# Kernel optimization log

Hardware: AMD Instinct MI355X
Metric: run time of the kernel (lower is better)

The kernel has to match this reference:

```python
import jax, jax.numpy as jnp
import numpy as np

HIDDEN, DOWN, UP, NH, RHD = 2048, 512, 1024, 16, 64
HEAD_DIM = HIDDEN // NH        # 128 (used only in the score scale)
V_HEAD = UP // NH              # 64
BASE = 10000.0


def _rope(q):
    # q: [bs, heads, seq, d] with even d. Faithful to the torch module,
    # including its swapped sin/cos cache names.
    d = q.shape[-1]
    seq = q.shape[2]
    theta = BASE ** (-jnp.arange(0, d, 2, dtype=jnp.float32) / d)      # [d/2]
    pos = jnp.arange(seq, dtype=jnp.float32)[:, None] * theta[None, :]  # [seq, d/2]
    cos_pos = jnp.repeat(jnp.sin(pos), 2, axis=-1)  # torch code: cos_pos = sin(...)
    sin_pos = jnp.repeat(jnp.cos(pos), 2, axis=-1)  # torch code: sin_pos = cos(...)
    q2 = jnp.stack([-q[..., 1::2], q[..., ::2]], axis=-1).reshape(q.shape)
    return q * cos_pos[None, None] + q2 * sin_pos[None, None]


def setup_inputs() -> dict:
    key = jax.random.key(0)
    ks = jax.random.split(key, 12)
    bs, seq = 16, 512

    def lin(k, fan_in, fan_out):
        kw, kb = jax.random.split(k)
        bound = 1.0 / np.sqrt(fan_in)
        W = jax.random.uniform(kw, (fan_in, fan_out), jnp.float32, -bound, bound)
        b = jax.random.uniform(kb, (fan_out,), jnp.float32, -bound, bound)
        return W, b

    x = jax.random.normal(ks[0], (bs, seq, HIDDEN), jnp.float32)
    mask = jax.random.randint(ks[1], (bs, seq), 0, 2, jnp.int32)
    w_dkv, b_dkv = lin(ks[2], HIDDEN, DOWN)
    w_dq, b_dq = lin(ks[3], HIDDEN, DOWN)
    w_uq, b_uq = lin(ks[4], DOWN, UP)
    w_uk, b_uk = lin(ks[5], DOWN, UP)
    w_uv, b_uv = lin(ks[6], DOWN, UP)
    w_qr, b_qr = lin(ks[7], DOWN, RHD * NH)
    w_kr, b_kr = lin(ks[8], DOWN, RHD)
    w_fc, b_fc = lin(ks[9], NH * V_HEAD, HIDDEN)
    return dict(x=x, mask=mask, w_dkv=w_dkv, b_dkv=b_dkv, w_dq=w_dq, b_dq=b_dq,
                w_uq=w_uq, b_uq=b_uq, w_uk=w_uk, b_uk=b_uk, w_uv=w_uv, b_uv=b_uv,
                w_qr=w_qr, b_qr=b_qr, w_kr=w_kr, b_kr=b_kr, w_fc=w_fc, b_fc=b_fc)


def reference(x, mask, w_dkv, b_dkv, w_dq, b_dq, w_uq, b_uq, w_uk, b_uk,
              w_uv, b_uv, w_qr, b_qr, w_kr, b_kr, w_fc, b_fc):
    bs, seq, _ = x.shape
    # latent down-projections
    c_kv = x @ w_dkv + b_dkv                       # [bs, seq, DOWN]
    c_q = x @ w_dq + b_dq                          # [bs, seq, DOWN]
    # content up-projections
    k_c = (c_kv @ w_uk + b_uk).reshape(bs, seq, NH, UP // NH).transpose(0, 2, 1, 3)
    v_c = (c_kv @ w_uv + b_uv).reshape(bs, seq, NH, V_HEAD).transpose(0, 2, 1, 3)
    q_c = (c_q @ w_uq + b_uq).reshape(bs, seq, NH, UP // NH).transpose(0, 2, 1, 3)
    # rope branches
    q_r = (c_q @ w_qr + b_qr).reshape(bs, seq, NH, RHD).transpose(0, 2, 1, 3)
    q_r = _rope(q_r)                               # [bs, NH, seq, RHD]
    k_r = (c_kv @ w_kr + b_kr)[:, None]            # [bs, 1, seq, RHD]
    k_r = _rope(k_r)
    # concat content + rope dims
    q = jnp.concatenate([q_c, q_r], axis=-1)                        # [bs,NH,seq,UP/NH+RHD]
    k = jnp.concatenate([k_c, jnp.broadcast_to(k_r, (bs, NH, seq, RHD))], axis=-1)
    scale = 1.0 / (HEAD_DIM ** 0.5 + RHD ** 0.5)
    scores = jnp.einsum('bhqd,bhkd->bhqk', q, k) * scale
    scores = jnp.where(mask[:, None, None, :] == 0, -jnp.inf, scores)
    attn = jax.nn.softmax(scores, axis=-1)
    ctx = jnp.einsum('bhqk,bhkd->bhqd', attn, v_c)                  # [bs,NH,seq,V_HEAD]
    ctx = ctx.transpose(0, 2, 1, 3).reshape(bs, seq, NH * V_HEAD)
    return ctx @ w_fc + b_fc
```

## Files before the change

kernel.cpp:

```cpp
#include <hip/hip_runtime.h>
#include <cstdint>
#include <cmath>

typedef unsigned short u16;
typedef unsigned int   u32;
typedef _Float16 f16x8 __attribute__((ext_vector_type(8)));
typedef float f32x4  __attribute__((ext_vector_type(4)));

#define MFMAH(a, b, c) __builtin_amdgcn_mfma_f32_16x16x32_f16((a), (b), (c), 0, 0, 0)

__device__ __forceinline__ u16 f2h(float f) {
  _Float16 h = (_Float16)f;
  return __builtin_bit_cast(u16, h);
}
__device__ __forceinline__ float h2f(u16 u) {
  return (float)__builtin_bit_cast(_Float16, u);
}
__device__ __forceinline__ float fexp2(float x) { return __builtin_amdgcn_exp2f(x); }
__device__ __forceinline__ void async16(const void* g, void* l) {
  __builtin_amdgcn_global_load_lds((const __attribute__((address_space(1))) u32*)g,
                                   (__attribute__((address_space(3))) u32*)l, 16, 0, 0);
}

__global__ void stab_kernel(float2* __restrict__ stab) {
  int idx = blockIdx.x * 256 + threadIdx.x;
  int s = idx >> 5, i = idx & 31;
  float theta = exp2f((float)i * (-13.287712379549449f / 32.0f));
  float ang = (float)s * theta;
  stab[idx] = make_float2(sinf(ang), cosf(ang));
}

__global__ void biascat_kernel(const float* __restrict__ buq, const float* __restrict__ bqr,
                               const float* __restrict__ buk, const float* __restrict__ buv,
                               const float* __restrict__ bkr,
                               float* __restrict__ biasQ, float* __restrict__ biasKV) {
  int idx = blockIdx.x * 256 + threadIdx.x;
  if (idx < 2048) biasQ[idx] = (idx < 1024) ? buq[idx] : bqr[idx - 1024];
  int j = idx - 2048;
  if (j >= 0 && j < 2176)
    biasKV[j] = (j < 1024) ? buk[j]
              : (j < 2048) ? buv[j - 1024]
              : (j < 2112) ? bkr[j - 2048] : 0.f;
}

__global__ void convert_x_kernel(const float* __restrict__ x, u16* __restrict__ xh, int n4) {
  int i = blockIdx.x * blockDim.x + threadIdx.x;
  if (i >= n4) return;
  float4 v = reinterpret_cast<const float4*>(x)[i];
  uint2 p;
  p.x = (u32)f2h(v.x) | ((u32)f2h(v.y) << 16);
  p.y = (u32)f2h(v.z) | ((u32)f2h(v.w) << 16);
  reinterpret_cast<uint2*>(xh)[i] = p;
}

template <int NOUT>
__global__ void wtrans_kernel(const float* __restrict__ W, int N,
                              u16* __restrict__ Thi, u16* __restrict__ Tlo,
                              int row_off, int dst_ld) {
  __shared__ float tile[32][33];
  int k0 = blockIdx.x * 32, n0 = blockIdx.y * 32;
  int tx = threadIdx.x & 31, ty = threadIdx.x >> 5;
#pragma unroll
  for (int i = 0; i < 32; i += 8)
    tile[ty + i][tx] = W[(size_t)(k0 + ty + i) * N + n0 + tx];
  __syncthreads();
#pragma unroll
  for (int i = 0; i < 32; i += 8) {
    float v = tile[tx][ty + i];
    size_t o = (size_t)(row_off + n0 + ty + i) * dst_ld + k0 + tx;
    u16 h = f2h(v);
    Thi[o] = h;
    if constexpr (NOUT == 2) Tlo[o] = f2h(v - h2f(h));
  }
}

template <int MODE, int TERMS>
__global__ __launch_bounds__(256, TERMS == 2 ? 3 : 4) void gemmh_kernel(
    const u16* __restrict__ Ah, int lda,
    const u16* __restrict__ Bhi, const u16* __restrict__ Blo, int ldb,
    const float* __restrict__ bias, const float* __restrict__ bias2, int bsplit,
    void* __restrict__ out0, void* __restrict__ out1, void* __restrict__ out2,
    const float2* __restrict__ stab, int N, int K, int ldc) {
  __shared__ u16 lA[128 * 64];
  __shared__ u16 lB[TERMS][128 * 64];
  const int tid = threadIdx.x;
  const int wave = tid >> 6, lane = tid & 63;
  const int lrow = lane & 15, kgrp = lane >> 4;
  const int nwg = gridDim.x * gridDim.y;
  const int orig = blockIdx.y * gridDim.x + blockIdx.x;
  const int swz = (orig & 7) * (nwg >> 3) + (orig >> 3);
  const int bm = (swz % gridDim.x) * 128, bn = (swz / gridDim.x) * 128;
  const int wm = (wave >> 1) * 64, wn = (wave & 1) * 64;
  const int srow = lane >> 3, sg = lane & 7;

  f32x4 acc[4][4];
  const f32x4 zero = {0.f, 0.f, 0.f, 0.f};
#pragma unroll
  for (int i = 0; i < 4; ++i)
#pragma unroll
    for (int j = 0; j < 4; ++j) acc[i][j] = zero;

  for (int kt = 0; kt < K; kt += 64) {
#pragma unroll
    for (int ii = 0; ii < 4; ++ii) {
      int inst = wave * 4 + ii;
      int row = inst * 8 + srow;
      int koff = kt + ((sg ^ (row & 7)) << 3);
      async16(Ah + (size_t)(bm + row) * lda + koff, &lA[inst * 512]);
      int brow = bn + row;
      if (brow > N - 1) brow = N - 1;
      async16(Bhi + (size_t)brow * ldb + koff, &lB[0][inst * 512]);
      if constexpr (TERMS == 2)
        async16(Blo + (size_t)brow * ldb + koff, &lB[TERMS - 1][inst * 512]);
    }
    asm volatile("s_waitcnt vmcnt(0)" ::: "memory");
    __syncthreads();

#pragma unroll
    for (int ks = 0; ks < 2; ++ks) {
      f16x8 ah[4], b0v[4], b1v[4];
#pragma unroll
      for (int mi = 0; mi < 4; ++mi) {
        int row = wm + mi * 16 + lrow;
        int off = row * 128 + ((ks * 64 + kgrp * 16) ^ ((row & 7) << 4));
        ah[mi] = *(const f16x8*)((const char*)lA + off);
      }
#pragma unroll
      for (int ni = 0; ni < 4; ++ni) {
        int row = wn + ni * 16 + lrow;
        int off = row * 128 + ((ks * 64 + kgrp * 16) ^ ((row & 7) << 4));
        b0v[ni] = *(const f16x8*)((const char*)lB[0] + off);
        if constexpr (TERMS == 2)
          b1v[ni] = *(const f16x8*)((const char*)lB[TERMS - 1] + off);
      }
#pragma unroll
      for (int mi = 0; mi < 4; ++mi)
#pragma unroll
        for (int ni = 0; ni < 4; ++ni) {
          acc[mi][ni] = MFMAH(ah[mi], b0v[ni], acc[mi][ni]);
          if constexpr (TERMS == 2)
            acc[mi][ni] = MFMAH(ah[mi], b1v[ni], acc[mi][ni]);
        }
    }
    __syncthreads();
  }

#pragma unroll
  for (int mi = 0; mi < 4; ++mi) {
#pragma unroll
    for (int ni = 0; ni < 4; ++ni) {
      int col = bn + wn + ni * 16 + lrow;
      float bv = (col < bsplit) ? bias[col] : bias2[col - bsplit];
      int row0 = bm + wm + mi * 16 + kgrp * 4;
      if constexpr (MODE == 0) {
#pragma unroll
        for (int r = 0; r < 4; ++r)
          ((float*)out0)[(size_t)(row0 + r) * ldc + col] = acc[mi][ni][r] + bv;
      } else if constexpr (MODE == 3) {
#pragma unroll
        for (int r = 0; r < 4; ++r)
          ((u16*)out0)[(size_t)(row0 + r) * ldc + col] = f2h(acc[mi][ni][r] + bv);
      } else if constexpr (MODE == 7) {
        if (col < 1024) {
#pragma unroll
          for (int r = 0; r < 4; ++r) {
            int row = row0 + r;
            ((u16*)out0)[(((size_t)((row >> 9) * 16 + (col >> 6)) * 512 + (row & 511)) << 7)
                         + (col & 63)] = f2h(acc[mi][ni][r] + bv);
          }
        } else {
          int cc = col - 1024, hh = cc >> 6, d = cc & 63, i2 = d >> 1;
          bool odd = d & 1;
#pragma unroll
          for (int r = 0; r < 4; ++r) {
            int row = row0 + r, s = row & 511;
            float vv = acc[mi][ni][r] + bv;
            float p = __shfl_xor(vv, 1, 64);
            float2 t2 = stab[s * 32 + i2];
            float o = odd ? (vv * t2.x + p * t2.y) : (vv * t2.x - p * t2.y);
            ((u16*)out0)[(((size_t)((row >> 9) * 16 + hh) * 512 + (row & 511)) << 7)
                         + 64 + d] = f2h(o);
          }
        }
      } else if constexpr (MODE == 6) {
        if (col < 1024) {
#pragma unroll
          for (int r = 0; r < 4; ++r) {
            int row = row0 + r;
            ((u16*)out0)[(((size_t)((row >> 9) * 16 + (col >> 6)) * 512 + (row & 511)) << 7)
                         + (col & 63)] = f2h(acc[mi][ni][r] + bv);
          }
        } else if (col < 2048) {
          int cc = col - 1024;
          u16 h0 = f2h(acc[mi][ni][0] + bv), h1 = f2h(acc[mi][ni][1] + bv);
          u16 h2 = f2h(acc[mi][ni][2] + bv), h3 = f2h(acc[mi][ni][3] + bv);
          uint2 pk;
          pk.x = (u32)h0 | ((u32)h1 << 16);
          pk.y = (u32)h2 | ((u32)h3 << 16);
          size_t base = ((size_t)((row0 >> 9) * 16 + (cc >> 6)) * 64 + (cc & 63)) * 512
                        + (row0 & 511);
          *reinterpret_cast<uint2*>((u16*)out1 + base) = pk;
        } else {
#pragma unroll
          for (int r = 0; r < 4; ++r)
            ((float*)out2)[(size_t)(row0 + r) * 128 + (col - 2048)] = acc[mi][ni][r] + bv;
        }
      }
    }
  }
}

__global__ void ropek_kernel(const float* __restrict__ kr, const float2* __restrict__ stab,
                             u16* __restrict__ Kb) {
  int idx = blockIdx.x * 256 + threadIdx.x;
  int t = idx >> 5, i = idx & 31;
  float vx = kr[(size_t)t * 128 + 2 * i], vy = kr[(size_t)t * 128 + 2 * i + 1];
  float2 t2 = stab[(t & 511) * 32 + i];
  float o0 = vx * t2.x - vy * t2.y;
  float o1 = vy * t2.x + vx * t2.y;
  u32 pk = (u32)f2h(o0) | ((u32)f2h(o1) << 16);
  int bb = t >> 9, ss = t & 511;
  size_t base = (size_t)bb * 16 * 512 * 128;
#pragma unroll
  for (int hh = 0; hh < 16; ++hh)
    *reinterpret_cast<u32*>(Kb + base + ((size_t)(hh * 512 + ss)) * 128 + 64 + 2 * i) = pk;
}

__global__ __launch_bounds__(256, 3) void attn_kernel(
    const u16* __restrict__ Qb, const u16* __restrict__ Kb, const u16* __restrict__ Vt,
    const int* __restrict__ mask, u16* __restrict__ ctx,
    float scale2) {
  __shared__ u16 sQ[64 * 128];
  __shared__ u16 sK[64 * 128];
  __shared__ u16 sV[64 * 64];
  __shared__ u16 sP[4][1024];
  const int tid = threadIdx.x, wave = tid >> 6, lane = tid & 63;
  const int lrow = lane & 15, kgrp = lane >> 4;
  const int bh = blockIdx.x, b = bh >> 4, h = bh & 15;
  const int q0 = blockIdx.y * 64;
  const size_t qkbase = (size_t)bh * 512 * 128;
  const size_t vbase = (size_t)bh * 64 * 512;
  u16* __restrict__ sPw = sP[wave];

  u32 poff[4][4];
#pragma unroll
  for (int r = 0; r < 4; ++r) {
    int qp = kgrp * 4 + r;
#pragma unroll
    for (int nf = 0; nf < 4; ++nf)
      poff[r][nf] = (u32)((nf >> 1) * 512 + ((((nf & 1) << 1) | (lrow >> 3))) * 128
                          + qp * 8 + (lrow & 7));
  }

  {
    int g = lane & 15, rr = lane >> 4;
#pragma unroll
    for (int ii = 0; ii < 4; ++ii) {
      int inst = wave * 4 + ii;
      int row = inst * 4 + rr;
      int perm = (g & 8) | ((g & 7) ^ (row & 7));
      async16(Qb + qkbase + (size_t)(q0 + row) * 128 + perm * 8, &sQ[inst * 512]);
    }
  }

  const f32x4 zero = {0.f, 0.f, 0.f, 0.f};
  f32x4 O[4];
#pragma unroll
  for (int nf = 0; nf < 4; ++nf) O[nf] = zero;
  float m_run[4], l_part[4];
#pragma unroll
  for (int r = 0; r < 4; ++r) { m_run[r] = -1e30f; l_part[r] = 0.f; }

  for (int kvt = 0; kvt < 8; ++kvt) {
    const int kv0 = kvt * 64;
    {
      int g = lane & 15, rr = lane >> 4;
#pragma unroll
      for (int ii = 0; ii < 4; ++ii) {
        int inst = wave * 4 + ii;
        int row = inst * 4 + rr;
        int perm = (g & 8) | ((g & 7) ^ (row & 7));
        async16(Kb + qkbase + (size_t)(kv0 + row) * 128 + perm * 8, &sK[inst * 512]);
      }
      int g2 = lane & 7, r2 = lane >> 3;
#pragma unroll
      for (int ii = 0; ii < 2; ++ii) {
        int inst = wave * 2 + ii;
        int row = inst * 8 + r2;
        async16(Vt + vbase + (size_t)row * 512 + kv0 + ((g2 ^ (row & 7)) << 3),
                &sV[inst * 512]);
      }
    }
    float mb[4];
#pragma unroll
    for (int nf = 0; nf < 4; ++nf)
      mb[nf] = (mask[b * 512 + kv0 + nf * 16 + lrow] != 0) ? 0.f : -1e30f;

    asm volatile("s_waitcnt vmcnt(0)" ::: "memory");
    __syncthreads();

    f32x4 S[4];
#pragma unroll
    for (int nf = 0; nf < 4; ++nf) S[nf] = zero;
#pragma unroll
    for (int ks = 0; ks < 4; ++ks) {
      int qrow = wave * 16 + lrow;
      int kb = ks * 64 + kgrp * 16;
      f16x8 aq = *(const f16x8*)((const char*)sQ + qrow * 256 + (kb ^ ((qrow & 7) << 4)));
#pragma unroll
      for (int nf = 0; nf < 4; ++nf) {
        int krow = nf * 16 + lrow;
        f16x8 bk = *(const f16x8*)((const char*)sK + krow * 256 + (kb ^ ((krow & 7) << 4)));
        S[nf] = MFMAH(aq, bk, S[nf]);
      }
    }

    float pvv[4][4];
    float tmax[4];
#pragma unroll
    for (int r = 0; r < 4; ++r) tmax[r] = -1e30f;
#pragma unroll
    for (int nf = 0; nf < 4; ++nf) {
#pragma unroll
      for (int r = 0; r < 4; ++r) {
        float v = fmaf(S[nf][r], scale2, mb[nf]);
        pvv[nf][r] = v;
        tmax[r] = fmaxf(tmax[r], v);
      }
    }
#pragma unroll
    for (int r = 0; r < 4; ++r) {
#pragma unroll
      for (int mv = 1; mv < 16; mv <<= 1)
        tmax[r] = fmaxf(tmax[r], __shfl_xor(tmax[r], mv, 64));
    }

    bool grow = (tmax[0] > m_run[0] + 8.f) || (tmax[1] > m_run[1] + 8.f) ||
                (tmax[2] > m_run[2] + 8.f) || (tmax[3] > m_run[3] + 8.f);
    if (__any(grow ? 1 : 0)) {
#pragma unroll
      for (int r = 0; r < 4; ++r) {
        float newm = fmaxf(m_run[r], tmax[r]);
        float sc = fexp2(m_run[r] - newm);
        m_run[r] = newm;
        float ts = 0.f;
#pragma unroll
        for (int nf = 0; nf < 4; ++nf) {
          float pe = fexp2(pvv[nf][r] - newm);
          sPw[poff[r][nf]] = f2h(pe);
          ts += pe;
        }
        l_part[r] = l_part[r] * sc + ts;
#pragma unroll
        for (int nf = 0; nf < 4; ++nf) O[nf][r] *= sc;
      }
    } else {
#pragma unroll
      for (int r = 0; r < 4; ++r) {
        float ts = 0.f;
#pragma unroll
        for (int nf = 0; nf < 4; ++nf) {
          float pe = fexp2(pvv[nf][r] - m_run[r]);
          sPw[poff[r][nf]] = f2h(pe);
          ts += pe;
        }
        l_part[r] += ts;
      }
    }

#pragma unroll
    for (int ks = 0; ks < 2; ++ks) {
      int kb = ks * 64 + kgrp * 16;
      f16x8 ap = *(const f16x8*)((const char*)sPw + ((ks * 64 + kgrp * 16 + lrow) << 4));
#pragma unroll
      for (int nf = 0; nf < 4; ++nf) {
        int vr = nf * 16 + lrow;
        f16x8 bv = *(const f16x8*)((const char*)sV + vr * 128 + (kb ^ ((vr & 7) << 4)));
        O[nf] = MFMAH(ap, bv, O[nf]);
      }
    }
    __syncthreads();
  }

#pragma unroll
  for (int r = 0; r < 4; ++r) {
#pragma unroll
    for (int mv = 1; mv < 16; mv <<= 1) l_part[r] += __shfl_xor(l_part[r], mv, 64);
  }

#pragma unroll
  for (int r = 0; r < 4; ++r) {
    float inv = 1.0f / l_part[r];
    int trow = b * 512 + q0 + wave * 16 + kgrp * 4 + r;
#pragma unroll
    for (int nf = 0; nf < 4; ++nf) {
      int col = h * 64 + nf * 16 + lrow;
      ctx[(size_t)trow * 1024 + col] = f2h(O[nf][r] * inv);
    }
  }
}

extern "C" void kernel_launch(void* const* d_in, const int* in_sizes, int n_in,
                              void* d_out, int out_size, void* d_ws, size_t ws_size,
                              hipStream_t stream) {
  const float* x     = (const float*)d_in[0];
  const int*   mask  = (const int*)d_in[1];
  const float* w_dkv = (const float*)d_in[2];
  const float* b_dkv = (const float*)d_in[3];
  const float* w_dq  = (const float*)d_in[4];
  const float* b_dq  = (const float*)d_in[5];
  const float* w_uq  = (const float*)d_in[6];
  const float* b_uq  = (const float*)d_in[7];
  const float* w_uk  = (const float*)d_in[8];
  const float* b_uk  = (const float*)d_in[9];
  const float* w_uv  = (const float*)d_in[10];
  const float* b_uv  = (const float*)d_in[11];
  const float* w_qr  = (const float*)d_in[12];
  const float* b_qr  = (const float*)d_in[13];
  const float* w_kr  = (const float*)d_in[14];
  const float* b_kr  = (const float*)d_in[15];
  const float* w_fc  = (const float*)d_in[16];
  const float* b_fc  = (const float*)d_in[17];
  float* out = (float*)d_out;

  char* ws = (char*)d_ws;
  size_t off = 0;
  auto alloc = [&](size_t bytes) -> void* {
    void* p = ws + off;
    off += (bytes + 255) & ~(size_t)255;
    return p;
  };
  u16* xh     = (u16*)alloc(33554432);
  u16* WfTh   = (u16*)alloc(4194304);
  u16* WfTl   = (u16*)alloc(4194304);
  u16* WqT    = (u16*)alloc(2097152);
  u16* WkvT   = (u16*)alloc(2228224);
  u16* WfcTh  = (u16*)alloc(4194304);
  u16* WfcTl  = (u16*)alloc(4194304);
  u16* c      = (u16*)alloc(16777216);
  u16* Qb     = (u16*)alloc(33554432);
  u16* Kb     = (u16*)alloc(33554432);
  u16* Vt     = (u16*)alloc(16777216);
  float* krf  = (float*)alloc(4194304);
  float2* stab = (float2*)alloc(131072);
  float* biasQ  = (float*)alloc(8192);
  float* biasKV = (float*)alloc(8704);
  u16* ctx = c;
  (void)ws_size; (void)in_sizes; (void)n_in; (void)out_size;

  const float scale = 1.0f / (sqrtf(128.0f) + sqrtf(64.0f));
  const float scale2 = scale * 1.4426950408889634f;

  stab_kernel<<<64, 256, 0, stream>>>(stab);
  convert_x_kernel<<<16384, 256, 0, stream>>>(x, xh, 4194304);
  biascat_kernel<<<17, 256, 0, stream>>>(b_uq, b_qr, b_uk, b_uv, b_kr, biasQ, biasKV);
  wtrans_kernel<2><<<dim3(64, 16), 256, 0, stream>>>(w_dkv, 512, WfTh, WfTl, 0, 2048);
  wtrans_kernel<2><<<dim3(64, 16), 256, 0, stream>>>(w_dq, 512, WfTh, WfTl, 512, 2048);
  wtrans_kernel<1><<<dim3(16, 32), 256, 0, stream>>>(w_uq, 1024, WqT, nullptr, 0, 512);
  wtrans_kernel<1><<<dim3(16, 32), 256, 0, stream>>>(w_qr, 1024, WqT, nullptr, 1024, 512);
  wtrans_kernel<1><<<dim3(16, 32), 256, 0, stream>>>(w_uk, 1024, WkvT, nullptr, 0, 512);
  wtrans_kernel<1><<<dim3(16, 32), 256, 0, stream>>>(w_uv, 1024, WkvT, nullptr, 1024, 512);
  wtrans_kernel<1><<<dim3(16, 2), 256, 0, stream>>>(w_kr, 64, WkvT, nullptr, 2048, 512);
  wtrans_kernel<2><<<dim3(32, 64), 256, 0, stream>>>(w_fc, 2048, WfcTh, WfcTl, 0, 1024);

  gemmh_kernel<3, 2><<<dim3(64, 8), 256, 0, stream>>>(
      xh, 2048, WfTh, WfTl, 2048, b_dkv, b_dq, 512,
      (void*)c, nullptr, nullptr, nullptr, 1024, 2048, 1024);
  gemmh_kernel<7, 1><<<dim3(64, 16), 256, 0, stream>>>(
      c + 512, 1024, WqT, nullptr, 512, biasQ, biasQ, 2048,
      (void*)Qb, nullptr, nullptr, stab, 2048, 512, 0);
  gemmh_kernel<6, 1><<<dim3(64, 17), 256, 0, stream>>>(
      c, 1024, WkvT, nullptr, 512, biasKV, biasKV, 2176,
      (void*)Kb, (void*)Vt, (void*)krf, nullptr, 2176, 512, 0);

  ropek_kernel<<<1024, 256, 0, stream>>>(krf, stab, Kb);

  attn_kernel<<<dim3(256, 8), 256, 0, stream>>>(Qb, Kb, Vt, mask, ctx, scale2);

  gemmh_kernel<0, 2><<<dim3(64, 16), 256, 0, stream>>>(
      ctx, 1024, WfcTh, WfcTl, 1024, b_fc, b_fc, 2048,
      (void*)out, nullptr, nullptr, nullptr, 2048, 1024, 2048);
}
```

Measured before the change: 458.7 us.

## Keep attention probabilities in registers via transposed S and batch prep launches

```diff
diff --git a/kernel.cpp b/kernel.cpp
--- a/kernel.cpp
+++ b/kernel.cpp
@@ -22,25 +22,25 @@
                                    (__attribute__((address_space(3))) u32*)l, 16, 0, 0);
 }
 
-__global__ void stab_kernel(float2* __restrict__ stab) {
+__global__ void prep_kernel(float2* __restrict__ stab,
+                            const float* __restrict__ buq, const float* __restrict__ bqr,
+                            const float* __restrict__ buk, const float* __restrict__ buv,
+                            const float* __restrict__ bkr,
+                            float* __restrict__ biasQ, float* __restrict__ biasKV) {
   int idx = blockIdx.x * 256 + threadIdx.x;
-  int s = idx >> 5, i = idx & 31;
-  float theta = exp2f((float)i * (-13.287712379549449f / 32.0f));
-  float ang = (float)s * theta;
-  stab[idx] = make_float2(sinf(ang), cosf(ang));
-}
-
-__global__ void biascat_kernel(const float* __restrict__ buq, const float* __restrict__ bqr,
-                               const float* __restrict__ buk, const float* __restrict__ buv,
-                               const float* __restrict__ bkr,
-                               float* __restrict__ biasQ, float* __restrict__ biasKV) {
-  int idx = blockIdx.x * 256 + threadIdx.x;
-  if (idx < 2048) biasQ[idx] = (idx < 1024) ? buq[idx] : bqr[idx - 1024];
-  int j = idx - 2048;
-  if (j >= 0 && j < 2176)
-    biasKV[j] = (j < 1024) ? buk[j]
-              : (j < 2048) ? buv[j - 1024]
-              : (j < 2112) ? bkr[j - 2048] : 0.f;
+  if (idx < 16384) {
+    int s = idx >> 5, i = idx & 31;
+    float theta = exp2f((float)i * (-13.287712379549449f / 32.0f));
+    float ang = (float)s * theta;
+    stab[idx] = make_float2(sinf(ang), cosf(ang));
+  }
+  int j = idx - 16384;
+  if (j >= 0 && j < 2048) biasQ[j] = (j < 1024) ? buq[j] : bqr[j - 1024];
+  int k = idx - 18432;
+  if (k >= 0 && k < 2176)
+    biasKV[k] = (k < 1024) ? buk[k]
+              : (k < 2048) ? buv[k - 1024]
+              : (k < 2112) ? bkr[k - 2048] : 0.f;
 }
 
 __global__ void convert_x_kernel(const float* __restrict__ x, u16* __restrict__ xh, int n4) {
@@ -53,11 +53,15 @@
   reinterpret_cast<uint2*>(xh)[i] = p;
 }
 
+struct Wptrs { const float* w0; const float* w1; const float* w2; const float* w3; };
 template <int NOUT>
-__global__ void wtrans_kernel(const float* __restrict__ W, int N,
+__global__ void wtrans_kernel(Wptrs wp, int N,
                               u16* __restrict__ Thi, u16* __restrict__ Tlo,
-                              int row_off, int dst_ld) {
+                              int row_off0, int row_stride, int dst_ld) {
   __shared__ float tile[32][33];
+  const float* W = (blockIdx.z == 0) ? wp.w0 : (blockIdx.z == 1) ? wp.w1
+                 : (blockIdx.z == 2) ? wp.w2 : wp.w3;
+  int row_off = row_off0 + blockIdx.z * row_stride;
   int k0 = blockIdx.x * 32, n0 = blockIdx.y * 32;
   int tx = threadIdx.x & 31, ty = threadIdx.x >> 5;
 #pragma unroll
@@ -194,12 +198,12 @@
           int cc = col - 1024;
           u16 h0 = f2h(acc[mi][ni][0] + bv), h1 = f2h(acc[mi][ni][1] + bv);
           u16 h2 = f2h(acc[mi][ni][2] + bv), h3 = f2h(acc[mi][ni][3] + bv);
-          uint2 pk;
-          pk.x = (u32)h0 | ((u32)h1 << 16);
-          pk.y = (u32)h2 | ((u32)h3 << 16);
+          uint2 pk2;
+          pk2.x = (u32)h0 | ((u32)h1 << 16);
+          pk2.y = (u32)h2 | ((u32)h3 << 16);
           size_t base = ((size_t)((row0 >> 9) * 16 + (cc >> 6)) * 64 + (cc & 63)) * 512
                         + (row0 & 511);
-          *reinterpret_cast<uint2*>((u16*)out1 + base) = pk;
+          *reinterpret_cast<uint2*>((u16*)out1 + base) = pk2;
         } else {
 #pragma unroll
           for (int r = 0; r < 4; ++r)
@@ -218,47 +222,35 @@
   float2 t2 = stab[(t & 511) * 32 + i];
   float o0 = vx * t2.x - vy * t2.y;
   float o1 = vy * t2.x + vx * t2.y;
-  u32 pk = (u32)f2h(o0) | ((u32)f2h(o1) << 16);
+  u32 pk2 = (u32)f2h(o0) | ((u32)f2h(o1) << 16);
   int bb = t >> 9, ss = t & 511;
   size_t base = (size_t)bb * 16 * 512 * 128;
 #pragma unroll
   for (int hh = 0; hh < 16; ++hh)
-    *reinterpret_cast<u32*>(Kb + base + ((size_t)(hh * 512 + ss)) * 128 + 64 + 2 * i) = pk;
-}
-
-__global__ __launch_bounds__(256, 3) void attn_kernel(
+    *reinterpret_cast<u32*>(Kb + base + ((size_t)(hh * 512 + ss)) * 128 + 64 + 2 * i) = pk2;
+}
+
+__global__ __launch_bounds__(256, 4) void attn_kernel(
     const u16* __restrict__ Qb, const u16* __restrict__ Kb, const u16* __restrict__ Vt,
     const int* __restrict__ mask, u16* __restrict__ ctx,
     float scale2) {
   __shared__ u16 sQ[64 * 128];
   __shared__ u16 sK[64 * 128];
   __shared__ u16 sV[64 * 64];
-  __shared__ u16 sP[4][1024];
   const int tid = threadIdx.x, wave = tid >> 6, lane = tid & 63;
-  const int lrow = lane & 15, kgrp = lane >> 4;
+  const int lrow = lane & 15, g = lane >> 4;
   const int bh = blockIdx.x, b = bh >> 4, h = bh & 15;
   const int q0 = blockIdx.y * 64;
   const size_t qkbase = (size_t)bh * 512 * 128;
   const size_t vbase = (size_t)bh * 64 * 512;
-  u16* __restrict__ sPw = sP[wave];
-
-  u32 poff[4][4];
-#pragma unroll
-  for (int r = 0; r < 4; ++r) {
-    int qp = kgrp * 4 + r;
-#pragma unroll
-    for (int nf = 0; nf < 4; ++nf)
-      poff[r][nf] = (u32)((nf >> 1) * 512 + ((((nf & 1) << 1) | (lrow >> 3))) * 128
-                          + qp * 8 + (lrow & 7));
-  }
 
   {
-    int g = lane & 15, rr = lane >> 4;
+    int gg = lane & 15, rr = lane >> 4;
 #pragma unroll
     for (int ii = 0; ii < 4; ++ii) {
       int inst = wave * 4 + ii;
       int row = inst * 4 + rr;
-      int perm = (g & 8) | ((g & 7) ^ (row & 7));
+      int perm = (gg & 8) | ((gg & 7) ^ (row & 7));
       async16(Qb + qkbase + (size_t)(q0 + row) * 128 + perm * 8, &sQ[inst * 512]);
     }
   }
@@ -267,19 +259,21 @@
   f32x4 O[4];
 #pragma unroll
   for (int nf = 0; nf < 4; ++nf) O[nf] = zero;
-  float m_run[4], l_part[4];
-#pragma unroll
-  for (int r = 0; r < 4; ++r) { m_run[r] = -1e30f; l_part[r] = 0.f; }
+  float m_run = -1e30f, lsum = 0.f;
+
+  const int laneA = lrow + ((lane & 16) << 1);
+  const int laneB = laneA + 16;
+  const bool sel = (lane & 32) != 0;
 
   for (int kvt = 0; kvt < 8; ++kvt) {
     const int kv0 = kvt * 64;
     {
-      int g = lane & 15, rr = lane >> 4;
+      int gg = lane & 15, rr = lane >> 4;
 #pragma unroll
       for (int ii = 0; ii < 4; ++ii) {
         int inst = wave * 4 + ii;
         int row = inst * 4 + rr;
-        int perm = (g & 8) | ((g & 7) ^ (row & 7));
+        int perm = (gg & 8) | ((gg & 7) ^ (row & 7));
         async16(Kb + qkbase + (size_t)(kv0 + row) * 128 + perm * 8, &sK[inst * 512]);
       }
       int g2 = lane & 7, r2 = lane >> 3;
@@ -291,10 +285,15 @@
                 &sV[inst * 512]);
       }
     }
-    float mb[4];
-#pragma unroll
-    for (int nf = 0; nf < 4; ++nf)
-      mb[nf] = (mask[b * 512 + kv0 + nf * 16 + lrow] != 0) ? 0.f : -1e30f;
+    float mb[4][4];
+#pragma unroll
+    for (int nf = 0; nf < 4; ++nf) {
+      int4 mk = *reinterpret_cast<const int4*>(&mask[b * 512 + kv0 + nf * 16 + g * 4]);
+      mb[nf][0] = mk.x ? 0.f : -1e30f;
+      mb[nf][1] = mk.y ? 0.f : -1e30f;
+      mb[nf][2] = mk.z ? 0.f : -1e30f;
+      mb[nf][3] = mk.w ? 0.f : -1e30f;
+    }
 
     asm volatile("s_waitcnt vmcnt(0)" ::: "memory");
     __syncthreads();
@@ -305,97 +304,105 @@
 #pragma unroll
     for (int ks = 0; ks < 4; ++ks) {
       int qrow = wave * 16 + lrow;
-      int kb = ks * 64 + kgrp * 16;
-      f16x8 aq = *(const f16x8*)((const char*)sQ + qrow * 256 + (kb ^ ((qrow & 7) << 4)));
+      int kb = ks * 64 + g * 16;
+      f16x8 bq = *(const f16x8*)((const char*)sQ + qrow * 256 + (kb ^ ((qrow & 7) << 4)));
 #pragma unroll
       for (int nf = 0; nf < 4; ++nf) {
         int krow = nf * 16 + lrow;
-        f16x8 bk = *(const f16x8*)((const char*)sK + krow * 256 + (kb ^ ((krow & 7) << 4)));
-        S[nf] = MFMAH(aq, bk, S[nf]);
+        f16x8 ak = *(const f16x8*)((const char*)sK + krow * 256 + (kb ^ ((krow & 7) << 4)));
+        S[nf] = MFMAH(ak, bq, S[nf]);
       }
     }
 
     float pvv[4][4];
-    float tmax[4];
-#pragma unroll
-    for (int r = 0; r < 4; ++r) tmax[r] = -1e30f;
+    float tm = -1e30f;
 #pragma unroll
     for (int nf = 0; nf < 4; ++nf) {
 #pragma unroll
       for (int r = 0; r < 4; ++r) {
-        float v = fmaf(S[nf][r], scale2, mb[nf]);
+        float v = fmaf(S[nf][r], scale2, mb[nf][r]);
         pvv[nf][r] = v;
-        tmax[r] = fmaxf(tmax[r], v);
-      }
-    }
-#pragma unroll
-    for (int r = 0; r < 4; ++r) {
-#pragma unroll
-      for (int mv = 1; mv < 16; mv <<= 1)
-        tmax[r] = fmaxf(tmax[r], __shfl_xor(tmax[r], mv, 64));
-    }
-
-    bool grow = (tmax[0] > m_run[0] + 8.f) || (tmax[1] > m_run[1] + 8.f) ||
-                (tmax[2] > m_run[2] + 8.f) || (tmax[3] > m_run[3] + 8.f);
+        tm = fmaxf(tm, v);
+      }
+    }
+    tm = fmaxf(tm, __shfl_xor(tm, 16, 64));
+    tm = fmaxf(tm, __shfl_xor(tm, 32, 64));
+
+    u32 pk[4][2];
+    float ts = 0.f;
+    bool grow = tm > m_run + 8.f;
     if (__any(grow ? 1 : 0)) {
-#pragma unroll
-      for (int r = 0; r < 4; ++r) {
-        float newm = fmaxf(m_run[r], tmax[r]);
-        float sc = fexp2(m_run[r] - newm);
-        m_run[r] = newm;
-        float ts = 0.f;
-#pragma unroll
-        for (int nf = 0; nf < 4; ++nf) {
-          float pe = fexp2(pvv[nf][r] - newm);
-          sPw[poff[r][nf]] = f2h(pe);
-          ts += pe;
-        }
-        l_part[r] = l_part[r] * sc + ts;
-#pragma unroll
-        for (int nf = 0; nf < 4; ++nf) O[nf][r] *= sc;
-      }
+      float newm = fmaxf(m_run, tm);
+      float sc = fexp2(m_run - newm);
+      m_run = newm;
+#pragma unroll
+      for (int nf = 0; nf < 4; ++nf) {
+        float e0 = fexp2(pvv[nf][0] - newm), e1 = fexp2(pvv[nf][1] - newm);
+        float e2 = fexp2(pvv[nf][2] - newm), e3 = fexp2(pvv[nf][3] - newm);
+        ts += (e0 + e1) + (e2 + e3);
+        pk[nf][0] = (u32)f2h(e0) | ((u32)f2h(e1) << 16);
+        pk[nf][1] = (u32)f2h(e2) | ((u32)f2h(e3) << 16);
+      }
+      lsum = lsum * sc + ts;
+      float scq[4];
+#pragma unroll
+      for (int r = 0; r < 4; ++r) scq[r] = __shfl(sc, g * 4 + r, 64);
+#pragma unroll
+      for (int nf = 0; nf < 4; ++nf)
+#pragma unroll
+        for (int r = 0; r < 4; ++r) O[nf][r] *= scq[r];
     } else {
 #pragma unroll
-      for (int r = 0; r < 4; ++r) {
-        float ts = 0.f;
-#pragma unroll
-        for (int nf = 0; nf < 4; ++nf) {
-          float pe = fexp2(pvv[nf][r] - m_run[r]);
-          sPw[poff[r][nf]] = f2h(pe);
-          ts += pe;
-        }
-        l_part[r] += ts;
-      }
+      for (int nf = 0; nf < 4; ++nf) {
+        float e0 = fexp2(pvv[nf][0] - m_run), e1 = fexp2(pvv[nf][1] - m_run);
+        float e2 = fexp2(pvv[nf][2] - m_run), e3 = fexp2(pvv[nf][3] - m_run);
+        ts += (e0 + e1) + (e2 + e3);
+        pk[nf][0] = (u32)f2h(e0) | ((u32)f2h(e1) << 16);
+        pk[nf][1] = (u32)f2h(e2) | ((u32)f2h(e3) << 16);
+      }
+      lsum += ts;
     }
 
 #pragma unroll
     for (int ks = 0; ks < 2; ++ks) {
-      int kb = ks * 64 + kgrp * 16;
-      f16x8 ap = *(const f16x8*)((const char*)sPw + ((ks * 64 + kgrp * 16 + lrow) << 4));
+      int n0 = 2 * ks, n1 = 2 * ks + 1;
+      u32 w0a = (u32)__shfl((int)pk[n0][0], laneA, 64);
+      u32 w0b = (u32)__shfl((int)pk[n1][0], laneA, 64);
+      u32 w1a = (u32)__shfl((int)pk[n0][1], laneA, 64);
+      u32 w1b = (u32)__shfl((int)pk[n1][1], laneA, 64);
+      u32 w2a = (u32)__shfl((int)pk[n0][0], laneB, 64);
+      u32 w2b = (u32)__shfl((int)pk[n1][0], laneB, 64);
+      u32 w3a = (u32)__shfl((int)pk[n0][1], laneB, 64);
+      u32 w3b = (u32)__shfl((int)pk[n1][1], laneB, 64);
+      union { u32 w[4]; f16x8 v; } ap;
+      ap.w[0] = sel ? w0b : w0a;
+      ap.w[1] = sel ? w1b : w1a;
+      ap.w[2] = sel ? w2b : w2a;
+      ap.w[3] = sel ? w3b : w3a;
+      int kb = ks * 64 + g * 16;
 #pragma unroll
       for (int nf = 0; nf < 4; ++nf) {
         int vr = nf * 16 + lrow;
         f16x8 bv = *(const f16x8*)((const char*)sV + vr * 128 + (kb ^ ((vr & 7) << 4)));
-        O[nf] = MFMAH(ap, bv, O[nf]);
+        O[nf] = MFMAH(ap.v, bv, O[nf]);
       }
     }
     __syncthreads();
   }
 
+  lsum += __shfl_xor(lsum, 16, 64);
+  lsum += __shfl_xor(lsum, 32, 64);
+  float linv[4];
+#pragma unroll
+  for (int r = 0; r < 4; ++r) linv[r] = 1.0f / __shfl(lsum, g * 4 + r, 64);
+
 #pragma unroll
   for (int r = 0; r < 4; ++r) {
-#pragma unroll
-    for (int mv = 1; mv < 16; mv <<= 1) l_part[r] += __shfl_xor(l_part[r], mv, 64);
-  }
-
-#pragma unroll
-  for (int r = 0; r < 4; ++r) {
-    float inv = 1.0f / l_part[r];
-    int trow = b * 512 + q0 + wave * 16 + kgrp * 4 + r;
+    int trow = b * 512 + q0 + wave * 16 + g * 4 + r;
 #pragma unroll
     for (int nf = 0; nf < 4; ++nf) {
       int col = h * 64 + nf * 16 + lrow;
-      ctx[(size_t)trow * 1024 + col] = f2h(O[nf][r] * inv);
+      ctx[(size_t)trow * 1024 + col] = f2h(O[nf][r] * linv[r]);
     }
   }
 }
@@ -451,17 +458,20 @@
   const float scale = 1.0f / (sqrtf(128.0f) + sqrtf(64.0f));
   const float scale2 = scale * 1.4426950408889634f;
 
-  stab_kernel<<<64, 256, 0, stream>>>(stab);
+  prep_kernel<<<81, 256, 0, stream>>>(stab, b_uq, b_qr, b_uk, b_uv, b_kr, biasQ, biasKV);
   convert_x_kernel<<<16384, 256, 0, stream>>>(x, xh, 4194304);
-  biascat_kernel<<<17, 256, 0, stream>>>(b_uq, b_qr, b_uk, b_uv, b_kr, biasQ, biasKV);
-  wtrans_kernel<2><<<dim3(64, 16), 256, 0, stream>>>(w_dkv, 512, WfTh, WfTl, 0, 2048);
-  wtrans_kernel<2><<<dim3(64, 16), 256, 0, stream>>>(w_dq, 512, WfTh, WfTl, 512, 2048);
-  wtrans_kernel<1><<<dim3(16, 32), 256, 0, stream>>>(w_uq, 1024, WqT, nullptr, 0, 512);
-  wtrans_kernel<1><<<dim3(16, 32), 256, 0, stream>>>(w_qr, 1024, WqT, nullptr, 1024, 512);
-  wtrans_kernel<1><<<dim3(16, 32), 256, 0, stream>>>(w_uk, 1024, WkvT, nullptr, 0, 512);
-  wtrans_kernel<1><<<dim3(16, 32), 256, 0, stream>>>(w_uv, 1024, WkvT, nullptr, 1024, 512);
-  wtrans_kernel<1><<<dim3(16, 2), 256, 0, stream>>>(w_kr, 64, WkvT, nullptr, 2048, 512);
-  wtrans_kernel<2><<<dim3(32, 64), 256, 0, stream>>>(w_fc, 2048, WfcTh, WfcTl, 0, 1024);
+  {
+    Wptrs wf{w_dkv, w_dq, nullptr, nullptr};
+    wtrans_kernel<2><<<dim3(64, 16, 2), 256, 0, stream>>>(wf, 512, WfTh, WfTl, 0, 512, 2048);
+    Wptrs wq{w_uq, w_qr, nullptr, nullptr};
+    wtrans_kernel<1><<<dim3(16, 32, 2), 256, 0, stream>>>(wq, 1024, WqT, nullptr, 0, 1024, 512);
+    Wptrs wkv{w_uk, w_uv, nullptr, nullptr};
+    wtrans_kernel<1><<<dim3(16, 32, 2), 256, 0, stream>>>(wkv, 1024, WkvT, nullptr, 0, 1024, 512);
+    Wptrs wkr{w_kr, nullptr, nullptr, nullptr};
+    wtrans_kernel<1><<<dim3(16, 2, 1), 256, 0, stream>>>(wkr, 64, WkvT, nullptr, 2048, 0, 512);
+    Wptrs wfc{w_fc, nullptr, nullptr, nullptr};
+    wtrans_kernel<2><<<dim3(32, 64, 1), 256, 0, stream>>>(wfc, 2048, WfcTh, WfcTl, 0, 0, 1024);
+  }
 
   gemmh_kernel<3, 2><<<dim3(64, 8), 256, 0, stream>>>(
       xh, 2048, WfTh, WfTl, 2048, b_dkv, b_dq, 512,
```

Measured after the change: 448.6 us. 2.2% less time.
